# Kernel tuning notes

Hardware: AMD Instinct MI355X
Metric: run time of the kernel (lower is better)

Reference implementation:

```python
import jax, jax.numpy as jnp
import numpy as np

LN_EPS = 1e-5

def _layernorm(x, g, b):
    mu = jnp.mean(x, axis=-1, keepdims=True)
    var = jnp.var(x, axis=-1, keepdims=True)
    return (x - mu) / jnp.sqrt(var + LN_EPS) * g + b

def setup_inputs() -> dict:
    key = jax.random.key(0)
    ks = jax.random.split(key, 12)
    N, D_WSI, D_OMIC, D, DH = 50000, 1024, 1577, 256, 128
    def rn(k, shape, s=0.02):
        return jax.random.normal(k, shape, jnp.float32) * s
    return {
        'wsi': jax.random.normal(ks[0], (N, D_WSI), jnp.float32),
        'x_omic': jax.random.normal(ks[1], (D_OMIC,), jnp.float32),
        # SNNOmics: Linear(1577,256)+ELU, Linear(256,256)+ELU (AlphaDropout=eval identity)
        'W1': rn(ks[2], (D_OMIC, 256)), 'b1': jnp.zeros((256,), jnp.float32),
        'W2': rn(ks[3], (256, 256)), 'b2': jnp.zeros((256,), jnp.float32),
        # wsi projection Linear(1024,256)
        'Wp': rn(ks[4], (D_WSI, D)), 'bp': jnp.zeros((D,), jnp.float32),
        # MMAttentionLayer pre-norm (dim=256)
        'ln1_g': jnp.ones((D,), jnp.float32), 'ln1_b': jnp.zeros((D,), jnp.float32),
        # to_qkv: Linear(256, 3*heads*dim_head) = Linear(256, 384), no bias (heads=1, dim_head=128)
        'Wqkv': rn(ks[5], (D, 3 * DH)),
        # FeedForward(dim=128, mult=1): LN + Linear(128,128)+GELU+Linear(128,128) (no residual)
        'ln2_g': jnp.ones((DH,), jnp.float32), 'ln2_b': jnp.zeros((DH,), jnp.float32),
        'Wf1': rn(ks[6], (DH, DH)), 'bf1': jnp.zeros((DH,), jnp.float32),
        'Wf2': rn(ks[7], (DH, DH)), 'bf2': jnp.zeros((DH,), jnp.float32),
        # final LayerNorm(128)
        'ln3_g': jnp.ones((DH,), jnp.float32), 'ln3_b': jnp.zeros((DH,), jnp.float32),
        # to_logits: Linear(256,64)+ReLU+Linear(64,4)
        'Wl1': rn(ks[8], (2 * DH, 64)), 'bl1': jnp.zeros((64,), jnp.float32),
        'Wl2': rn(ks[9], (64, 4)), 'bl2': jnp.zeros((4,), jnp.float32),
    }

def reference(wsi, x_omic, W1, b1, W2, b2, Wp, bp, ln1_g, ln1_b, Wqkv,
              ln2_g, ln2_b, Wf1, bf1, Wf2, bf2, ln3_g, ln3_b, Wl1, bl1, Wl2, bl2):
    M = 1            # num_pathways
    DH = 128         # dim_head (heads=1)
    scale = DH ** -0.5
    # SNN omics encoder -> one pathway token [1, 256]
    h = jax.nn.elu(x_omic @ W1 + b1)
    h = jax.nn.elu(h @ W2 + b2)
    h_omic = h[None, :]                              # [1, 256]
    # WSI projection -> histology tokens [N, 256]
    wsi_embed = wsi @ Wp + bp                        # [N, 256]
    tokens = jnp.concatenate([h_omic, wsi_embed], axis=0)   # [1+N, 256]
    # MMAttentionLayer: pre-norm then asymmetric pathway/histology attention
    xn = _layernorm(tokens, ln1_g, ln1_b)
    qkv = xn @ Wqkv                                  # [1+N, 384]
    q, k, v = jnp.split(qkv, 3, axis=-1)             # each [1+N, 128]
    q = q * scale
    q_p, q_h = q[:M], q[M:]                          # [1,128], [N,128]
    k_p, k_h = k[:M], k[M:]
    # cross attention: histology -> pathways (rows of length M=1)
    cross_attn_hist = q_h @ k_p.T                    # [N, 1]
    cross_attn_hist = jax.nn.softmax(cross_attn_hist, axis=-1)
    # pathway row attends to [pathways | histology]
    attn_p = q_p @ k_p.T                             # [1, 1]
    cross_attn_p = q_p @ k_h.T                       # [1, N]
    attn_ph = jax.nn.softmax(jnp.concatenate([attn_p, cross_attn_p], axis=-1), axis=-1)  # [1, 1+N]
    out_p = attn_ph @ v                              # [1, 128]
    out_h = cross_attn_hist @ v[:M]                  # [N, 128]
    out = jnp.concatenate([out_p, out_h], axis=0)    # [1+N, 128] (residual=False: no conv)
    # FeedForward (no residual add in original) + LayerNorm
    mm = _layernorm(out, ln2_g, ln2_b)
    mm = jax.nn.gelu(mm @ Wf1 + bf1, approximate=False) @ Wf2 + bf2
    mm = _layernorm(mm, ln3_g, ln3_b)                # [1+N, 128]
    paths_embed = jnp.mean(mm[:M], axis=0)           # [128]
    wsi_embed_post = jnp.mean(mm[M:], axis=0)        # [128]
    embedding = jnp.concatenate([paths_embed, wsi_embed_post])[None, :]  # [1, 256]
    logits = jax.nn.relu(embedding @ Wl1 + bl1) @ Wl2 + bl2              # [1, 4]
    prob = jax.nn.softmax(logits, axis=-1)
    return logits, prob
```

## Files before the change

kernel.cpp:

```cpp
#include <hip/hip_runtime.h>
#include <hip/hip_bf16.h>
#include <math.h>

#define LN_EPS 1e-5f

typedef unsigned short ushortT;
typedef short bf16x8 __attribute__((ext_vector_type(8)));
typedef float f32x4 __attribute__((ext_vector_type(4)));

#define WS_QP   0
#define WS_V0   128
#define WS_S0   256
#define WS_LL   258
#define WS_E0   259
#define WS_H1P  512
#define WS_PART 4608
#define PART_STRIDE 132
#define PART_M 128
#define PART_L 129
#define WS_WTS  108000
#define WS_GP   109000
#define NCOMB   32
#define WS_WPT  131072
#define WS_WKVT 262144

__device__ __forceinline__ float elu1(float x){ return x > 0.f ? x : expm1f(x); }
__device__ __forceinline__ unsigned pk2(float lo, float hi){
  union { __hip_bfloat162 h; unsigned u; } cv;
  cv.h = __float22bfloat162_rn(make_float2(lo, hi));
  return cv.u;
}
__device__ __forceinline__ void dma16(const void* g, void* l) {
  __builtin_amdgcn_global_load_lds(
      (const __attribute__((address_space(1))) unsigned int*)g,
      (__attribute__((address_space(3))) unsigned int*)l, 16, 0, 0);
}
template<int N> __device__ __forceinline__ void vwait() {
  asm volatile("s_waitcnt vmcnt(%0)" :: "i"(N) : "memory");
}
__device__ __forceinline__ void lwait0() {
  asm volatile("s_waitcnt lgkmcnt(0)" ::: "memory");
}
__device__ __forceinline__ void sbar()   { __builtin_amdgcn_s_barrier(); }
__device__ __forceinline__ void schedb() { __builtin_amdgcn_sched_barrier(0); }

__global__ __launch_bounds__(256) void k_setup(
    const float* __restrict__ Wp, const float* __restrict__ Wqkv,
    const float* __restrict__ x, const float* __restrict__ W1, int d_omic,
    ushortT* __restrict__ wpt, ushortT* __restrict__ wkvt, float* __restrict__ ws)
{
  int bb = blockIdx.x, t = threadIdx.x;
  if (bb < 32) {
    int kc = bb, m = t, sw = (m >> 1) & 3;
    #pragma unroll
    for (int c = 0; c < 4; ++c) {
      float v[8];
      #pragma unroll
      for (int e = 0; e < 8; ++e) v[e] = Wp[(size_t)(kc * 32 + c * 8 + e) * 256 + m];
      uint4 w = make_uint4(pk2(v[0], v[1]), pk2(v[2], v[3]), pk2(v[4], v[5]), pk2(v[6], v[7]));
      *(uint4*)&wpt[kc * 8192 + m * 32 + ((c ^ sw) * 8)] = w;
    }
  } else if (bb < 40) {
    int kk = bb - 32, m = t, sw = (m >> 1) & 3;
    #pragma unroll
    for (int c = 0; c < 4; ++c) {
      float v[8];
      #pragma unroll
      for (int e = 0; e < 8; ++e) v[e] = Wqkv[(size_t)(kk * 32 + c * 8 + e) * 384 + 128 + m];
      uint4 w = make_uint4(pk2(v[0], v[1]), pk2(v[2], v[3]), pk2(v[4], v[5]), pk2(v[6], v[7]));
      *(uint4*)&wkvt[kk * 8192 + m * 32 + ((c ^ sw) * 8)] = w;
    }
  } else {
    int g = bb - 40;
    int i0 = g * 99, i1 = min(i0 + 99, d_omic);
    __shared__ float xs[112];
    for (int i = i0 + t; i < i1; i += 256) xs[i - i0] = x[i];
    __syncthreads();
    float s = 0.f;
    for (int i = i0; i < i1; i++) s = fmaf(xs[i - i0], W1[(size_t)i * 256 + t], s);
    ws[WS_H1P + g * 256 + t] = s;
  }
}

__global__ __launch_bounds__(256) void k_omic(
    const float* __restrict__ b1,
    const float* __restrict__ W2, const float* __restrict__ b2,
    const float* __restrict__ Wqkv,
    const float* __restrict__ ln1_g, const float* __restrict__ ln1_b,
    float* __restrict__ ws)
{
  __shared__ float h1[256];
  __shared__ float xn0[256];
  __shared__ float qs[128], ks[128];
  __shared__ float red[8];
  int tid = threadIdx.x, lane = tid & 63, wave = tid >> 6;

  float s = b1[tid];
  for (int g = 0; g < 16; g++) s += ws[WS_H1P + g * 256 + tid];
  h1[tid] = elu1(s);
  __syncthreads();

  s = b2[tid];
  for (int i = 0; i < 256; i++) s = fmaf(h1[i], W2[i * 256 + tid], s);
  float t0 = elu1(s);

  float ps = t0, pq = t0 * t0;
  for (int m = 1; m < 64; m <<= 1) { ps += __shfl_xor(ps, m); pq += __shfl_xor(pq, m); }
  if (lane == 0) { red[wave] = ps; red[4 + wave] = pq; }
  __syncthreads();
  float mu = (red[0] + red[1] + red[2] + red[3]) * (1.f / 256.f);
  float var = (red[4] + red[5] + red[6] + red[7]) * (1.f / 256.f) - mu * mu;
  float xn = (t0 - mu) * rsqrtf(var + LN_EPS) * ln1_g[tid] + ln1_b[tid];
  xn0[tid] = xn;
  __syncthreads();

  float a = 0.f;
  for (int j = 0; j < 256; j++) a = fmaf(xn0[j], Wqkv[j * 384 + tid], a);
  if (tid < 128) { float q = a * 0.088388347648318447f; qs[tid] = q; ws[WS_QP + tid] = q; }
  else           { ks[tid - 128] = a; }
  if (tid < 128) {
    float av = 0.f;
    for (int j = 0; j < 256; j++) av = fmaf(xn0[j], Wqkv[j * 384 + 256 + tid], av);
    ws[WS_V0 + tid] = av;
  }
  __syncthreads();
  float p = (tid < 128) ? qs[tid] * ks[tid] : 0.f;
  for (int m = 1; m < 64; m <<= 1) p += __shfl_xor(p, m);
  if (lane == 0) red[wave] = p;
  __syncthreads();
  if (tid == 0) ws[WS_S0] = red[0] + red[1] + red[2] + red[3];
}

__global__ __launch_bounds__(512, 4) void k_main(
    const float* __restrict__ wsi, int N,
    const ushortT* __restrict__ wpt, const ushortT* __restrict__ wkvt,
    const float* __restrict__ bp,
    const float* __restrict__ ln1_g, const float* __restrict__ ln1_b,
    float* __restrict__ ws)
{
  __shared__ __align__(16) char U[65536];
  char* Uw = U + 32768;

  const int tid = threadIdx.x;
  const int lane = tid & 63, wv = tid >> 6;
  const int l15 = lane & 15, lh = lane >> 4;
  const int cg = wv & 3, rg = wv >> 2;
  const int b = blockIdx.x, r0 = b * 128;

  int wsiSrc[2];
  #pragma unroll
  for (int i = 0; i < 2; ++i) {
    int rowL = 16 * wv + 8 * i + (lane >> 3);
    int gr = r0 + rowL; gr = (gr < N) ? gr : (N - 1);
    wsiSrc[i] = gr * 1024 + (((lane & 7) ^ (lane >> 3)) << 2);
  }
  int wptSrc[2];
  #pragma unroll
  for (int j = 0; j < 2; ++j) wptSrc[j] = (32 * wv + 16 * j) * 32 + lane * 8;

  const unsigned afslot = (unsigned)((lh ^ ((l15 >> 1) & 3)) << 4);
  const unsigned bs0 = (unsigned)(((2 * lh)     ^ (l15 & 7)) << 4);
  const unsigned bs1 = (unsigned)(((2 * lh + 1) ^ (l15 & 7)) << 4);

  const f32x4 z4 = {0.f, 0.f, 0.f, 0.f};
  f32x4 acc[4][4];
  #pragma unroll
  for (int mt = 0; mt < 4; ++mt)
    #pragma unroll
    for (int nt = 0; nt < 4; ++nt) acc[mt][nt] = z4;

  auto dmaSlice = [&](int kc, int k) {
    char* ds = U + k * 16384 + wv * 2048;
    #pragma unroll
    for (int i = 0; i < 2; ++i) dma16(wsi + wsiSrc[i] + kc * 32, ds + i * 1024);
    char* dw = Uw + k * 16384 + wv * 2048;
    #pragma unroll
    for (int j = 0; j < 2; ++j) dma16(wpt + wptSrc[j] + kc * 8192, dw + j * 1024);
  };

  dmaSlice(0, 0);
  for (int s = 0; s < 32; ++s) {
    if (s < 31) { dmaSlice(s + 1, (s + 1) & 1); vwait<4>(); }
    else vwait<0>();
    sbar(); schedb();
    {
      const char* Ws = U  + (s & 1) * 16384;
      const char* Wf = Uw + (s & 1) * 16384;
      bf16x8 af[4], bfr[4];
      #pragma unroll
      for (int mt = 0; mt < 4; ++mt)
        af[mt] = *(const bf16x8*)(Wf + (64 * cg + 16 * mt + l15) * 64 + afslot);
      #pragma unroll
      for (int nt = 0; nt < 4; ++nt) {
        const char* p = Ws + (64 * rg + 16 * nt + l15) * 128;
        uint4 ua = *(const uint4*)(p + bs0);
        uint4 ub = *(const uint4*)(p + bs1);
        union { unsigned u[4]; bf16x8 v; } cv;
        cv.u[0] = pk2(__uint_as_float(ua.x), __uint_as_float(ua.y));
        cv.u[1] = pk2(__uint_as_float(ua.z), __uint_as_float(ua.w));
        cv.u[2] = pk2(__uint_as_float(ub.x), __uint_as_float(ub.y));
        cv.u[3] = pk2(__uint_as_float(ub.z), __uint_as_float(ub.w));
        bfr[nt] = cv.v;
      }
      #pragma unroll
      for (int mt = 0; mt < 4; ++mt)
        #pragma unroll
        for (int nt = 0; nt < 4; ++nt)
          acc[mt][nt] = __builtin_amdgcn_mfma_f32_16x16x32_bf16(af[mt], bfr[nt], acc[mt][nt], 0, 0, 0);
    }
    sbar(); schedb();
  }

  float* red = (float*)U;
  float4 bp4[4], g4[4], b4[4];
  #pragma unroll
  for (int mt = 0; mt < 4; ++mt) {
    int m0 = 64 * cg + 16 * mt + 4 * lh;
    bp4[mt] = *(const float4*)&bp[m0];
    g4[mt]  = *(const float4*)&ln1_g[m0];
    b4[mt]  = *(const float4*)&ln1_b[m0];
  }
  float ps[4], pq[4];
  #pragma unroll
  for (int nt = 0; nt < 4; ++nt) { ps[nt] = 0.f; pq[nt] = 0.f; }
  #pragma unroll
  for (int mt = 0; mt < 4; ++mt) {
    const float bb4[4] = {bp4[mt].x, bp4[mt].y, bp4[mt].z, bp4[mt].w};
    #pragma unroll
    for (int nt = 0; nt < 4; ++nt)
      #pragma unroll
      for (int r = 0; r < 4; ++r) {
        float v = acc[mt][nt][r] + bb4[r];
        acc[mt][nt][r] = v;
        ps[nt] += v; pq[nt] += v * v;
      }
  }
  #pragma unroll
  for (int nt = 0; nt < 4; ++nt) {
    ps[nt] += __shfl_xor(ps[nt], 16); pq[nt] += __shfl_xor(pq[nt], 16);
    ps[nt] += __shfl_xor(ps[nt], 32); pq[nt] += __shfl_xor(pq[nt], 32);
  }
  if (lh == 0) {
    #pragma unroll
    for (int nt = 0; nt < 4; ++nt) {
      int row = 64 * rg + 16 * nt + l15;
      *(float2*)&red[row * 8 + cg * 2] = make_float2(ps[nt], pq[nt]);
    }
  }
  lwait0(); sbar(); schedb();
  float mu[4], rstd[4];
  #pragma unroll
  for (int nt = 0; nt < 4; ++nt) {
    int row = 64 * rg + 16 * nt + l15;
    float s_ = 0.f, q_ = 0.f;
    #pragma unroll
    for (int c = 0; c < 4; ++c) { s_ += red[row * 8 + c * 2]; q_ += red[row * 8 + c * 2 + 1]; }
    float m_ = s_ * (1.f / 256.f);
    float v_ = q_ * (1.f / 256.f) - m_ * m_;
    mu[nt] = m_; rstd[nt] = rsqrtf(v_ + LN_EPS);
  }
  lwait0(); sbar(); schedb();

  #pragma unroll
  for (int nt = 0; nt < 4; ++nt) {
    int row = 64 * rg + 16 * nt + l15;
    unsigned rswz = (unsigned)((row & 7) << 4);
    #pragma unroll
    for (int mt = 0; mt < 4; ++mt) {
      float x0 = (acc[mt][nt][0] - mu[nt]) * rstd[nt] * g4[mt].x + b4[mt].x;
      float x1 = (acc[mt][nt][1] - mu[nt]) * rstd[nt] * g4[mt].y + b4[mt].y;
      float x2 = (acc[mt][nt][2] - mu[nt]) * rstd[nt] * g4[mt].z + b4[mt].z;
      float x3 = (acc[mt][nt][3] - mu[nt]) * rstd[nt] * g4[mt].w + b4[mt].w;
      unsigned off = (unsigned)(row * 512 + (64 * cg + 16 * mt + 4 * lh) * 2) ^ rswz;
      *(uint2*)(U + off) = make_uint2(pk2(x0, x1), pk2(x2, x3));
    }
  }
  lwait0(); sbar(); schedb();

  f32x4 acc2[4][4];
  #pragma unroll
  for (int mt = 0; mt < 4; ++mt)
    #pragma unroll
    for (int nt = 0; nt < 4; ++nt) acc2[mt][nt] = z4;
  int kvBase[4];
  #pragma unroll
  for (int mt = 0; mt < 4; ++mt) {
    int m = 64 * cg + 16 * mt + l15;
    kvBase[mt] = m * 32 + ((lh ^ ((m >> 1) & 3)) << 3);
  }
  bf16x8 gA[4], gB[4];
  #pragma unroll
  for (int mt = 0; mt < 4; ++mt) gA[mt] = *(const bf16x8*)(wkvt + kvBase[mt]);
  #pragma unroll
  for (int kp = 0; kp < 4; ++kp) {
    const int kk0 = 2 * kp, kk1 = 2 * kp + 1;
    #pragma unroll
    for (int mt = 0; mt < 4; ++mt)
      gB[mt] = *(const bf16x8*)(wkvt + kvBase[mt] + kk1 * 8192);
    {
      bf16x8 bfr[4];
      #pragma unroll
      for (int nt = 0; nt < 4; ++nt) {
        int row = 64 * rg + 16 * nt + l15;
        unsigned off = (unsigned)(row * 512 + kk0 * 64 + lh * 16) ^ (unsigned)((row & 7) << 4);
        bfr[nt] = *(const bf16x8*)(U + off);
      }
      #pragma unroll
      for (int mt = 0; mt < 4; ++mt)
        #pragma unroll
        for (int nt = 0; nt < 4; ++nt)
          acc2[mt][nt] = __builtin_amdgcn_mfma_f32_16x16x32_bf16(gA[mt], bfr[nt], acc2[mt][nt], 0, 0, 0);
    }
    if (kp < 3) {
      #pragma unroll
      for (int mt = 0; mt < 4; ++mt)
        gA[mt] = *(const bf16x8*)(wkvt + kvBase[mt] + (kk0 + 2) * 8192);
    }
    {
      bf16x8 bfr[4];
      #pragma unroll
      for (int nt = 0; nt < 4; ++nt) {
        int row = 64 * rg + 16 * nt + l15;
        unsigned off = (unsigned)(row * 512 + kk1 * 64 + lh * 16) ^ (unsigned)((row & 7) << 4);
        bfr[nt] = *(const bf16x8*)(U + off);
      }
      #pragma unroll
      for (int mt = 0; mt < 4; ++mt)
        #pragma unroll
        for (int nt = 0; nt < 4; ++nt)
          acc2[mt][nt] = __builtin_amdgcn_mfma_f32_16x16x32_bf16(gB[mt], bfr[nt], acc2[mt][nt], 0, 0, 0);
    }
  }
  sbar(); schedb();

  float* sred = (float*)U;
  float* aux  = (float*)(U + 1024);
  float* wts  = (float*)(U + 1056);
  float* vred = (float*)(U + 1600);
  float* part = ws + WS_PART + (size_t)b * PART_STRIDE;

  if (cg < 2) {
    float4 qp4[4];
    #pragma unroll
    for (int mt = 0; mt < 4; ++mt)
      qp4[mt] = *(const float4*)&ws[WS_QP + 64 * cg + 16 * mt + 4 * lh];
    float sp[4];
    #pragma unroll
    for (int nt = 0; nt < 4; ++nt) {
      float s_ = 0.f;
      #pragma unroll
      for (int mt = 0; mt < 4; ++mt) {
        s_ = fmaf(qp4[mt].x, acc2[mt][nt][0], s_);
        s_ = fmaf(qp4[mt].y, acc2[mt][nt][1], s_);
        s_ = fmaf(qp4[mt].z, acc2[mt][nt][2], s_);
        s_ = fmaf(qp4[mt].w, acc2[mt][nt][3], s_);
      }
      sp[nt] = s_;
    }
    #pragma unroll
    for (int nt = 0; nt < 4; ++nt) {
      sp[nt] += __shfl_xor(sp[nt], 16);
      sp[nt] += __shfl_xor(sp[nt], 32);
    }
    if (lh == 0) {
      #pragma unroll
      for (int nt = 0; nt < 4; ++nt) sred[cg * 128 + 64 * rg + 16 * nt + l15] = sp[nt];
    }
  }
  lwait0(); sbar(); schedb();

  float sv = -INFINITY, ev = 0.f;
  if (tid < 128) {
    sv = sred[tid] + sred[128 + tid];
    if (r0 + tid >= N) sv = -INFINITY;
  }
  float mb = sv;
  #pragma unroll
  for (int m = 1; m < 64; m <<= 1) mb = fmaxf(mb, __shfl_xor(mb, m));
  if (tid < 128 && lane == 0) aux[tid >> 6] = mb;
  lwait0(); sbar(); schedb();
  float M2 = fmaxf(aux[0], aux[1]);
  if (tid < 128) { ev = (r0 + tid < N) ? expf(sv - M2) : 0.f; wts[tid] = ev; }
  float lsum = ev;
  #pragma unroll
  for (int m = 1; m < 64; m <<= 1) lsum += __shfl_xor(lsum, m);
  if (tid < 128 && lane == 0) aux[2 + (tid >> 6)] = lsum;
  lwait0(); sbar(); schedb();
  if (tid == 0) { part[PART_M] = M2; part[PART_L] = aux[2] + aux[3]; }

  if (cg >= 2) {
    float wr[4];
    #pragma unroll
    for (int nt = 0; nt < 4; ++nt) wr[nt] = wts[64 * rg + 16 * nt + l15];
    #pragma unroll
    for (int mt = 0; mt < 4; ++mt) {
      float vs0 = 0.f, vs1 = 0.f, vs2 = 0.f, vs3 = 0.f;
      #pragma unroll
      for (int nt = 0; nt < 4; ++nt) {
        vs0 = fmaf(wr[nt], acc2[mt][nt][0], vs0);
        vs1 = fmaf(wr[nt], acc2[mt][nt][1], vs1);
        vs2 = fmaf(wr[nt], acc2[mt][nt][2], vs2);
        vs3 = fmaf(wr[nt], acc2[mt][nt][3], vs3);
      }
      #pragma unroll
      for (int m = 1; m < 16; m <<= 1) {
        vs0 += __shfl_xor(vs0, m); vs1 += __shfl_xor(vs1, m);
        vs2 += __shfl_xor(vs2, m); vs3 += __shfl_xor(vs3, m);
      }
      if (l15 == 0)
        *(float4*)&vred[128 * rg + 64 * (cg - 2) + 16 * mt + 4 * lh] =
            make_float4(vs0, vs1, vs2, vs3);
    }
  }
  lwait0(); sbar(); schedb();
  if (tid < 128) part[tid] = vred[tid] + vred[128 + tid];
}

__global__ __launch_bounds__(256) void k_fin0(float* __restrict__ ws, int NB)
{
  __shared__ float red[8];
  int tid = threadIdx.x, lane = tid & 63, wave = tid >> 6;
  const float* part = ws + WS_PART;
  float s0 = ws[WS_S0];

  float mloc = s0;
  for (int bb = tid; bb < NB; bb += 256) mloc = fmaxf(mloc, part[(size_t)bb * PART_STRIDE + PART_M]);
  for (int m = 1; m < 64; m <<= 1) mloc = fmaxf(mloc, __shfl_xor(mloc, m));
  if (lane == 0) red[wave] = mloc;
  __syncthreads();
  float M = fmaxf(fmaxf(red[0], red[1]), fmaxf(red[2], red[3]));

  float lp = 0.f;
  for (int bb = tid; bb < NB; bb += 256) {
    float w = expf(part[(size_t)bb * PART_STRIDE + PART_M] - M);
    ws[WS_WTS + bb] = w;
    lp = fmaf(part[(size_t)bb * PART_STRIDE + PART_L], w, lp);
  }
  for (int m = 1; m < 64; m <<= 1) lp += __shfl_xor(lp, m);
  __syncthreads();
  if (lane == 0) red[wave] = lp;
  __syncthreads();
  if (tid == 0) {
    float e0 = expf(s0 - M);
    ws[WS_LL] = red[0] + red[1] + red[2] + red[3] + e0;
    ws[WS_E0] = e0;
  }
}

__global__ __launch_bounds__(128) void k_fin1(float* __restrict__ ws, int NB, int chunk)
{
  int g = blockIdx.x, col = threadIdx.x;
  int c0 = g * chunk, c1 = min(c0 + chunk, NB);
  const float* part = ws + WS_PART;
  const float* wts = ws + WS_WTS;
  float a = 0.f;
  #pragma unroll 4
  for (int bb = c0; bb < c1; ++bb)
    a = fmaf(part[(size_t)bb * PART_STRIDE + col], wts[bb], a);
  ws[WS_GP + g * 128 + col] = a;
}

__global__ __launch_bounds__(256) void k_final(
    const float* __restrict__ ws,
    const float* __restrict__ Wf1, const float* __restrict__ bf1,
    const float* __restrict__ Wf2, const float* __restrict__ bf2,
    const float* __restrict__ ln2_g, const float* __restrict__ ln2_b,
    const float* __restrict__ ln3_g, const float* __restrict__ ln3_b,
    const float* __restrict__ Wl1, const float* __restrict__ bl1,
    const float* __restrict__ Wl2, const float* __restrict__ bl2,
    float* __restrict__ out)
{
  __shared__ float rowb[2][128];
  __shared__ float mmb[2][128];
  __shared__ float red[8];
  __shared__ float emb[256];
  __shared__ float abuf[64];
  __shared__ float lbuf[4];
  int tid = threadIdx.x, lane = tid & 63, wave = tid >> 6;

  if (tid < 128) {
    float v0 = ws[WS_V0 + tid];
    float a = v0 * ws[WS_E0];
    #pragma unroll
    for (int g = 0; g < NCOMB; ++g) a += ws[WS_GP + g * 128 + tid];
    rowb[0][tid] = a / ws[WS_LL];
    rowb[1][tid] = v0;
  }
  __syncthreads();

  int row = tid >> 7, k = tid & 127;
  float x = rowb[row][k];
  float ps = x, pq = x * x;
  for (int m = 1; m < 64; m <<= 1) { ps += __shfl_xor(ps, m); pq += __shfl_xor(pq, m); }
  __syncthreads();
  if (lane == 0) { red[wave] = ps; red[4 + wave] = pq; }
  __syncthreads();
  {
    float sum = red[row * 2] + red[row * 2 + 1];
    float sq  = red[4 + row * 2] + red[4 + row * 2 + 1];
    float mu = sum * (1.f / 128.f);
    float var = sq * (1.f / 128.f) - mu * mu;
    x = (x - mu) * rsqrtf(var + LN_EPS) * ln2_g[k] + ln2_b[k];
  }
  mmb[row][k] = x;
  __syncthreads();
  float t1 = bf1[k];
  for (int j = 0; j < 128; j++) t1 = fmaf(mmb[row][j], Wf1[j * 128 + k], t1);
  float gg = t1 * 0.5f * (1.f + erff(t1 * 0.70710678118654752f));
  __syncthreads();
  rowb[row][k] = gg;
  __syncthreads();
  float t2 = bf2[k];
  for (int j = 0; j < 128; j++) t2 = fmaf(rowb[row][j], Wf2[j * 128 + k], t2);
  ps = t2; pq = t2 * t2;
  for (int m = 1; m < 64; m <<= 1) { ps += __shfl_xor(ps, m); pq += __shfl_xor(pq, m); }
  __syncthreads();
  if (lane == 0) { red[wave] = ps; red[4 + wave] = pq; }
  __syncthreads();
  {
    float sum = red[row * 2] + red[row * 2 + 1];
    float sq  = red[4 + row * 2] + red[4 + row * 2 + 1];
    float mu = sum * (1.f / 128.f);
    float var = sq * (1.f / 128.f) - mu * mu;
    t2 = (t2 - mu) * rsqrtf(var + LN_EPS) * ln3_g[k] + ln3_b[k];
  }
  emb[row * 128 + k] = t2;
  __syncthreads();
  if (tid < 64) {
    float a = bl1[tid];
    for (int j = 0; j < 256; j++) a = fmaf(emb[j], Wl1[j * 64 + tid], a);
    abuf[tid] = fmaxf(a, 0.f);
  }
  __syncthreads();
  if (tid < 4) {
    float lg = bl2[tid];
    for (int j = 0; j < 64; j++) lg = fmaf(abuf[j], Wl2[j * 4 + tid], lg);
    lbuf[tid] = lg;
  }
  __syncthreads();
  if (tid < 4) {
    float m4 = fmaxf(fmaxf(lbuf[0], lbuf[1]), fmaxf(lbuf[2], lbuf[3]));
    float e0 = expf(lbuf[0] - m4), e1 = expf(lbuf[1] - m4);
    float e2 = expf(lbuf[2] - m4), e3 = expf(lbuf[3] - m4);
    float ssum = e0 + e1 + e2 + e3;
    out[tid] = lbuf[tid];
    out[4 + tid] = expf(lbuf[tid] - m4) / ssum;
  }
}

extern "C" void kernel_launch(void* const* d_in, const int* in_sizes, int n_in,
                              void* d_out, int out_size, void* d_ws, size_t ws_size,
                              hipStream_t stream) {
  const float* wsi    = (const float*)d_in[0];
  const float* x_omic = (const float*)d_in[1];
  const float* W1     = (const float*)d_in[2];
  const float* b1     = (const float*)d_in[3];
  const float* W2     = (const float*)d_in[4];
  const float* b2     = (const float*)d_in[5];
  const float* Wp     = (const float*)d_in[6];
  const float* bp     = (const float*)d_in[7];
  const float* ln1_g  = (const float*)d_in[8];
  const float* ln1_b  = (const float*)d_in[9];
  const float* Wqkv   = (const float*)d_in[10];
  const float* ln2_g  = (const float*)d_in[11];
  const float* ln2_b  = (const float*)d_in[12];
  const float* Wf1    = (const float*)d_in[13];
  const float* bf1    = (const float*)d_in[14];
  const float* Wf2    = (const float*)d_in[15];
  const float* bf2    = (const float*)d_in[16];
  const float* ln3_g  = (const float*)d_in[17];
  const float* ln3_b  = (const float*)d_in[18];
  const float* Wl1    = (const float*)d_in[19];
  const float* bl1    = (const float*)d_in[20];
  const float* Wl2    = (const float*)d_in[21];
  const float* bl2    = (const float*)d_in[22];
  float* ws   = (float*)d_ws;
  float* outp = (float*)d_out;
  ushortT* wpt  = (ushortT*)(ws + WS_WPT);
  ushortT* wkvt = (ushortT*)(ws + WS_WKVT);

  int N = in_sizes[0] / 1024;
  int d_omic = in_sizes[1];
  int NB = (N + 127) / 128;
  int chunk = (NB + NCOMB - 1) / NCOMB;

  k_setup<<<56, 256, 0, stream>>>(Wp, Wqkv, x_omic, W1, d_omic, wpt, wkvt, ws);
  k_omic<<<1, 256, 0, stream>>>(b1, W2, b2, Wqkv, ln1_g, ln1_b, ws);
  k_main<<<NB, 512, 0, stream>>>(wsi, N, wpt, wkvt, bp, ln1_g, ln1_b, ws);
  k_fin0<<<1, 256, 0, stream>>>(ws, NB);
  k_fin1<<<NCOMB, 128, 0, stream>>>(ws, NB, chunk);
  k_final<<<1, 256, 0, stream>>>(ws, Wf1, bf1, Wf2, bf2, ln2_g, ln2_b,
                                 ln3_g, ln3_b, Wl1, bl1, Wl2, bl2, outp);
}
```

Before: 131.8 us.

## Double k_main row tile to 256 and fold global softmax merge into fin kernels

k_main now processes 256 wsi rows per block with 1024 threads and 128 KB of LDS. Each staged Wp bf16 slice is shared by twice as many rows, which cuts the Wp staging traffic per row. The separate k_fin0 pass is removed: k_fin1 does a local online-softmax merge per chunk (chunk max and rescaled sums), and k_final merges the NCOMB chunk maxima. This saves one launch and one serial pass, but leaves fewer, larger blocks (about 196 for the 256 CUs) and allows only one block per CU because of the LDS size.

```diff
diff --git a/kernel.cpp b/kernel.cpp
--- a/kernel.cpp
+++ b/kernel.cpp
@@ -11,15 +11,13 @@
 #define WS_QP   0
 #define WS_V0   128
 #define WS_S0   256
-#define WS_LL   258
-#define WS_E0   259
 #define WS_H1P  512
 #define WS_PART 4608
 #define PART_STRIDE 132
 #define PART_M 128
 #define PART_L 129
-#define WS_WTS  108000
 #define WS_GP   109000
+#define GP_STRIDE 132
 #define NCOMB   32
 #define WS_WPT  131072
 #define WS_WKVT 262144
@@ -131,21 +129,20 @@
   if (tid == 0) ws[WS_S0] = red[0] + red[1] + red[2] + red[3];
 }
 
-__global__ __launch_bounds__(512, 4) void k_main(
+__global__ __launch_bounds__(1024, 4) void k_main(
     const float* __restrict__ wsi, int N,
     const ushortT* __restrict__ wpt, const ushortT* __restrict__ wkvt,
     const float* __restrict__ bp,
     const float* __restrict__ ln1_g, const float* __restrict__ ln1_b,
     float* __restrict__ ws)
 {
-  __shared__ __align__(16) char U[65536];
-  char* Uw = U + 32768;
+  __shared__ __align__(16) char U[131072];
 
   const int tid = threadIdx.x;
   const int lane = tid & 63, wv = tid >> 6;
   const int l15 = lane & 15, lh = lane >> 4;
   const int cg = wv & 3, rg = wv >> 2;
-  const int b = blockIdx.x, r0 = b * 128;
+  const int b = blockIdx.x, r0 = b * 256;
 
   int wsiSrc[2];
   #pragma unroll
@@ -154,9 +151,7 @@
     int gr = r0 + rowL; gr = (gr < N) ? gr : (N - 1);
     wsiSrc[i] = gr * 1024 + (((lane & 7) ^ (lane >> 3)) << 2);
   }
-  int wptSrc[2];
-  #pragma unroll
-  for (int j = 0; j < 2; ++j) wptSrc[j] = (32 * wv + 16 * j) * 32 + lane * 8;
+  const int wptSrc = (16 * wv) * 32 + lane * 8;
 
   const unsigned afslot = (unsigned)((lh ^ ((l15 >> 1) & 3)) << 4);
   const unsigned bs0 = (unsigned)(((2 * lh)     ^ (l15 & 7)) << 4);
@@ -170,22 +165,21 @@
     for (int nt = 0; nt < 4; ++nt) acc[mt][nt] = z4;
 
   auto dmaSlice = [&](int kc, int k) {
-    char* ds = U + k * 16384 + wv * 2048;
+    char* ds = U + k * 32768 + wv * 2048;
     #pragma unroll
     for (int i = 0; i < 2; ++i) dma16(wsi + wsiSrc[i] + kc * 32, ds + i * 1024);
-    char* dw = Uw + k * 16384 + wv * 2048;
-    #pragma unroll
-    for (int j = 0; j < 2; ++j) dma16(wpt + wptSrc[j] + kc * 8192, dw + j * 1024);
+    char* dw = U + 65536 + k * 16384 + wv * 1024;
+    dma16(wpt + wptSrc + kc * 8192, dw);
   };
 
   dmaSlice(0, 0);
   for (int s = 0; s < 32; ++s) {
-    if (s < 31) { dmaSlice(s + 1, (s + 1) & 1); vwait<4>(); }
+    if (s < 31) { dmaSlice(s + 1, (s + 1) & 1); vwait<3>(); }
     else vwait<0>();
     sbar(); schedb();
     {
-      const char* Ws = U  + (s & 1) * 16384;
-      const char* Wf = Uw + (s & 1) * 16384;
+      const char* Ws = U + (s & 1) * 32768;
+      const char* Wf = U + 65536 + (s & 1) * 16384;
       bf16x8 af[4], bfr[4];
       #pragma unroll
       for (int mt = 0; mt < 4; ++mt)
@@ -211,7 +205,7 @@
     sbar(); schedb();
   }
 
-  float* red = (float*)U;
+  float* red = (float*)(U + 98304);
   float4 bp4[4], g4[4], b4[4];
   #pragma unroll
   for (int mt = 0; mt < 4; ++mt) {
@@ -334,9 +328,9 @@
   sbar(); schedb();
 
   float* sred = (float*)U;
-  float* aux  = (float*)(U + 1024);
-  float* wts  = (float*)(U + 1056);
-  float* vred = (float*)(U + 1600);
+  float* aux  = (float*)(U + 2048);
+  float* wts  = (float*)(U + 2112);
+  float* vred = (float*)(U + 3200);
   float* part = ws + WS_PART + (size_t)b * PART_STRIDE;
 
   if (cg < 2) {
@@ -364,29 +358,29 @@
     }
     if (lh == 0) {
       #pragma unroll
-      for (int nt = 0; nt < 4; ++nt) sred[cg * 128 + 64 * rg + 16 * nt + l15] = sp[nt];
+      for (int nt = 0; nt < 4; ++nt) sred[cg * 256 + 64 * rg + 16 * nt + l15] = sp[nt];
     }
   }
   lwait0(); sbar(); schedb();
 
   float sv = -INFINITY, ev = 0.f;
-  if (tid < 128) {
-    sv = sred[tid] + sred[128 + tid];
+  if (tid < 256) {
+    sv = sred[tid] + sred[256 + tid];
     if (r0 + tid >= N) sv = -INFINITY;
   }
   float mb = sv;
   #pragma unroll
   for (int m = 1; m < 64; m <<= 1) mb = fmaxf(mb, __shfl_xor(mb, m));
-  if (tid < 128 && lane == 0) aux[tid >> 6] = mb;
-  lwait0(); sbar(); schedb();
-  float M2 = fmaxf(aux[0], aux[1]);
-  if (tid < 128) { ev = (r0 + tid < N) ? expf(sv - M2) : 0.f; wts[tid] = ev; }
+  if (tid < 256 && lane == 0) aux[tid >> 6] = mb;
+  lwait0(); sbar(); schedb();
+  float M2 = fmaxf(fmaxf(aux[0], aux[1]), fmaxf(aux[2], aux[3]));
+  if (tid < 256) { ev = (r0 + tid < N) ? expf(sv - M2) : 0.f; wts[tid] = ev; }
   float lsum = ev;
   #pragma unroll
   for (int m = 1; m < 64; m <<= 1) lsum += __shfl_xor(lsum, m);
-  if (tid < 128 && lane == 0) aux[2 + (tid >> 6)] = lsum;
-  lwait0(); sbar(); schedb();
-  if (tid == 0) { part[PART_M] = M2; part[PART_L] = aux[2] + aux[3]; }
+  if (tid < 256 && lane == 0) aux[4 + (tid >> 6)] = lsum;
+  lwait0(); sbar(); schedb();
+  if (tid == 0) { part[PART_M] = M2; part[PART_L] = aux[4] + aux[5] + aux[6] + aux[7]; }
 
   if (cg >= 2) {
     float wr[4];
@@ -413,38 +407,8 @@
     }
   }
   lwait0(); sbar(); schedb();
-  if (tid < 128) part[tid] = vred[tid] + vred[128 + tid];
-}
-
-__global__ __launch_bounds__(256) void k_fin0(float* __restrict__ ws, int NB)
-{
-  __shared__ float red[8];
-  int tid = threadIdx.x, lane = tid & 63, wave = tid >> 6;
-  const float* part = ws + WS_PART;
-  float s0 = ws[WS_S0];
-
-  float mloc = s0;
-  for (int bb = tid; bb < NB; bb += 256) mloc = fmaxf(mloc, part[(size_t)bb * PART_STRIDE + PART_M]);
-  for (int m = 1; m < 64; m <<= 1) mloc = fmaxf(mloc, __shfl_xor(mloc, m));
-  if (lane == 0) red[wave] = mloc;
-  __syncthreads();
-  float M = fmaxf(fmaxf(red[0], red[1]), fmaxf(red[2], red[3]));
-
-  float lp = 0.f;
-  for (int bb = tid; bb < NB; bb += 256) {
-    float w = expf(part[(size_t)bb * PART_STRIDE + PART_M] - M);
-    ws[WS_WTS + bb] = w;
-    lp = fmaf(part[(size_t)bb * PART_STRIDE + PART_L], w, lp);
-  }
-  for (int m = 1; m < 64; m <<= 1) lp += __shfl_xor(lp, m);
-  __syncthreads();
-  if (lane == 0) red[wave] = lp;
-  __syncthreads();
-  if (tid == 0) {
-    float e0 = expf(s0 - M);
-    ws[WS_LL] = red[0] + red[1] + red[2] + red[3] + e0;
-    ws[WS_E0] = e0;
-  }
+  if (tid < 128)
+    part[tid] = vred[tid] + vred[128 + tid] + vred[256 + tid] + vred[384 + tid];
 }
 
 __global__ __launch_bounds__(128) void k_fin1(float* __restrict__ ws, int NB, int chunk)
@@ -452,12 +416,20 @@
   int g = blockIdx.x, col = threadIdx.x;
   int c0 = g * chunk, c1 = min(c0 + chunk, NB);
   const float* part = ws + WS_PART;
-  const float* wts = ws + WS_WTS;
-  float a = 0.f;
-  #pragma unroll 4
+  float mg = -INFINITY;
   for (int bb = c0; bb < c1; ++bb)
-    a = fmaf(part[(size_t)bb * PART_STRIDE + col], wts[bb], a);
-  ws[WS_GP + g * 128 + col] = a;
+    mg = fmaxf(mg, part[(size_t)bb * PART_STRIDE + PART_M]);
+  float a = 0.f, lg = 0.f;
+  for (int bb = c0; bb < c1; ++bb) {
+    float w = expf(part[(size_t)bb * PART_STRIDE + PART_M] - mg);
+    a  = fmaf(part[(size_t)bb * PART_STRIDE + col], w, a);
+    lg = fmaf(part[(size_t)bb * PART_STRIDE + PART_L], w, lg);
+  }
+  ws[WS_GP + g * GP_STRIDE + col] = a;
+  if (col == 0) {
+    ws[WS_GP + g * GP_STRIDE + 128] = mg;
+    ws[WS_GP + g * GP_STRIDE + 129] = lg;
+  }
 }
 
 __global__ __launch_bounds__(256) void k_final(
@@ -476,14 +448,30 @@
   __shared__ float emb[256];
   __shared__ float abuf[64];
   __shared__ float lbuf[4];
+  __shared__ float wg[NCOMB];
+  __shared__ float MLs[2];
   int tid = threadIdx.x, lane = tid & 63, wave = tid >> 6;
+  float s0 = ws[WS_S0];
+
+  if (tid == 0) {
+    float M = s0;
+    for (int g = 0; g < NCOMB; ++g) M = fmaxf(M, ws[WS_GP + g * GP_STRIDE + 128]);
+    float L = expf(s0 - M);
+    for (int g = 0; g < NCOMB; ++g)
+      L = fmaf(ws[WS_GP + g * GP_STRIDE + 129], expf(ws[WS_GP + g * GP_STRIDE + 128] - M), L);
+    MLs[0] = M; MLs[1] = L;
+  }
+  __syncthreads();
+  float M = MLs[0], L = MLs[1];
+  if (tid < NCOMB) wg[tid] = expf(ws[WS_GP + tid * GP_STRIDE + 128] - M);
+  __syncthreads();
 
   if (tid < 128) {
     float v0 = ws[WS_V0 + tid];
-    float a = v0 * ws[WS_E0];
-    #pragma unroll
-    for (int g = 0; g < NCOMB; ++g) a += ws[WS_GP + g * 128 + tid];
-    rowb[0][tid] = a / ws[WS_LL];
+    float a = v0 * expf(s0 - M);
+    #pragma unroll
+    for (int g = 0; g < NCOMB; ++g) a = fmaf(ws[WS_GP + g * GP_STRIDE + tid], wg[g], a);
+    rowb[0][tid] = a / L;
     rowb[1][tid] = v0;
   }
   __syncthreads();
@@ -581,13 +569,12 @@
 
   int N = in_sizes[0] / 1024;
   int d_omic = in_sizes[1];
-  int NB = (N + 127) / 128;
+  int NB = (N + 255) / 256;
   int chunk = (NB + NCOMB - 1) / NCOMB;
 
   k_setup<<<56, 256, 0, stream>>>(Wp, Wqkv, x_omic, W1, d_omic, wpt, wkvt, ws);
   k_omic<<<1, 256, 0, stream>>>(b1, W2, b2, Wqkv, ln1_g, ln1_b, ws);
-  k_main<<<NB, 512, 0, stream>>>(wsi, N, wpt, wkvt, bp, ln1_g, ln1_b, ws);
-  k_fin0<<<1, 256, 0, stream>>>(ws, NB);
+  k_main<<<NB, 1024, 0, stream>>>(wsi, N, wpt, wkvt, bp, ln1_g, ln1_b, ws);
   k_fin1<<<NCOMB, 128, 0, stream>>>(ws, NB, chunk);
   k_final<<<1, 256, 0, stream>>>(ws, Wf1, bf1, Wf2, bf2, ln2_g, ln2_b,
                                  ln3_g, ln3_b, Wl1, bl1, Wl2, bl2, outp);
```

New measurement: 141.2 us. +7.1%, slower.
